# Optimization experiments

Hardware: AMD Instinct MI355X
Metric: run time of the kernel (lower is better)

The kernel has to match this reference:

```python
import jax, jax.numpy as jnp
import numpy as np

_SAMPLING_EPS = 1e-5
NEG_INF = jnp.float32(-jnp.inf)


def setup_inputs() -> dict:
    key = jax.random.key(0)
    k1, k2, k3, k4, k5 = jax.random.split(key, 5)
    B, V = 128, 128000
    logits = jax.random.normal(k1, (B, V), dtype=jnp.float32) * 4.0
    # every 8th row is greedy (temperature 0), rest random in [0.1, 1.5)
    rand_t = 0.1 + 1.4 * jax.random.uniform(k2, (B,), dtype=jnp.float32)
    temperatures = jnp.where(jnp.arange(B) % 8 == 0, 0.0, rand_t)
    top_k = jax.random.randint(k3, (B,), 1, 1001, dtype=jnp.int64)
    top_p = 0.1 + 0.9 * jax.random.uniform(k4, (B,), dtype=jnp.float32)
    # q ~ Exponential(1), replaces torch's generator-based q.exponential_()
    exp_noise = jax.random.exponential(k5, (B, V), dtype=jnp.float32)
    return {"logits": logits, "temperatures": temperatures, "top_k": top_k,
            "top_p": top_p, "exp_noise": exp_noise}


def _masked_logits(logits, temperatures, top_k, top_p):
    B, V = logits.shape
    # apply_temperature: greedy rows (temp < eps) divide by 1.0
    temp = jnp.where(temperatures < _SAMPLING_EPS, 1.0, temperatures)
    x = logits / temp[:, None]                       # [B, V]
    # ascending sort (as in torch code)
    sort_idx = jnp.argsort(x, axis=-1)               # [B, V]
    x_sort = jnp.take_along_axis(x, sort_idx, axis=-1)
    # top-k: keep the k largest (last k of ascending sort)
    k = jnp.clip(top_k, None, V).astype(jnp.int32)
    thr_idx = (V - k)[:, None]                       # [B, 1]
    thr = jnp.take_along_axis(x_sort, thr_idx, axis=-1)
    x_sort = jnp.where(x_sort < thr, NEG_INF, x_sort)
    # top-p on the sorted (ascending) logits
    probs_sort = jax.nn.softmax(x_sort, axis=-1)
    probs_sum = jnp.cumsum(probs_sort, axis=-1)
    p_mask = probs_sum <= (1.0 - top_p)[:, None]
    p_mask = p_mask.at[:, -1].set(False)             # always keep the max
    x_sort = jnp.where(p_mask, NEG_INF, x_sort)
    # scatter back to original positions: out[b, sort_idx[b, j]] = x_sort[b, j]
    rows = jnp.arange(B)[:, None]
    return x.at[rows, sort_idx].set(x_sort)


def reference(logits, temperatures, top_k, top_p, exp_noise):
    logits = logits.astype(jnp.float32)
    greedy = jnp.argmax(logits, axis=-1)             # [B]
    masked = _masked_logits(logits, temperatures, top_k, top_p)
    probs = jax.nn.softmax(masked, axis=-1)
    # Gumbel-max / exponential-race sampling: argmax(probs / q)
    random_sampled = jnp.argmax(probs / exp_noise, axis=-1)
    sampled = jnp.where(temperatures < _SAMPLING_EPS, greedy, random_sampled)
    return sampled[:, None].astype(jnp.int32)        # SamplerOutput.sampled_token_ids
```

## Files before the change

kernel.cpp:

```cpp
#include <hip/hip_runtime.h>
#include <stdint.h>

#define HB 4096
#define CAP 4096
#define SL1 5
#define SL3 20
#define THR1 256
#define THR4 1024
#define SEPS 1e-5f
#define ZMAX 8
#define LBUF 2048

typedef unsigned long long ull;

__device__ __forceinline__ uint32_t f2key(float x) {
  uint32_t u = __float_as_uint(x);
  return u ^ ((u & 0x80000000u) ? 0xFFFFFFFFu : 0x80000000u);
}
__device__ __forceinline__ float key2f(uint32_t k) {
  uint32_t u = (k & 0x80000000u) ? (k ^ 0x80000000u) : ~k;
  return __uint_as_float(u);
}

__global__ void k1_hist(const float* __restrict__ logits, const float* __restrict__ noise,
                        const float* __restrict__ temps,
                        unsigned int* __restrict__ hist, ull* __restrict__ rowmax,
                        unsigned int* __restrict__ zcnt, int* __restrict__ zlist,
                        int V, int slice_len) {
  __shared__ unsigned int h[HB];
  __shared__ ull s_w64[THR1 / 64];
  int tid = threadIdx.x;
  int row = blockIdx.x / SL1;
  int slice = blockIdx.x % SL1;
  for (int b = tid; b < HB; b += THR1) h[b] = 0;
  __syncthreads();
  float tr = temps[row];
  float te = (tr < SEPS) ? 1.0f : tr;
  int col_base = slice * slice_len;
  const float4* p4 = reinterpret_cast<const float4*>(logits + (size_t)row * V + col_base);
  const float4* q4 = reinterpret_cast<const float4*>(noise + (size_t)row * V + col_base);
  int n4 = slice_len >> 2;
  ull best = 0ULL;
  for (int v = tid; v < n4; v += THR1) {
    float4 f = p4[v];
    float4 q = q4[v];
    int c0 = col_base + 4 * v;
    float xs[4] = {f.x, f.y, f.z, f.w};
    float qs[4] = {q.x, q.y, q.z, q.w};
#pragma unroll
    for (int m = 0; m < 4; ++m) {
      float x = xs[m] / te;
      uint32_t key = f2key(x);
      if (key >= 0x80000000u)
        atomicAdd(&h[(key & 0x7FFFFFFFu) >> 19], 1u);
      ull pk = ((ull)key << 32) | (ull)(uint32_t)(V - 1 - (c0 + m));
      if (pk > best) best = pk;
      if (qs[m] == 0.0f) {
        unsigned int p = atomicAdd(&zcnt[row], 1u);
        if (p < ZMAX) zlist[row * ZMAX + p] = c0 + m;
      }
    }
  }
  for (int off = 32; off > 0; off >>= 1) {
    ull o = __shfl_down(best, off);
    if (o > best) best = o;
  }
  int lane = tid & 63, wid = tid >> 6;
  if (lane == 0) s_w64[wid] = best;
  __syncthreads();
  if (tid == 0) {
    ull b2 = s_w64[0];
    for (int w = 1; w < THR1 / 64; ++w) if (s_w64[w] > b2) b2 = s_w64[w];
    atomicMax(&rowmax[row], b2);
  }
  for (int b = tid; b < HB; b += THR1) {
    unsigned int c = h[b];
    if (c) atomicAdd(&hist[(size_t)row * HB + b], c);
  }
}

__global__ void k2_select(const unsigned int* __restrict__ hist, const int* __restrict__ topk32,
                          unsigned int* __restrict__ tcap, int* __restrict__ kks, int B, int V) {
  __shared__ int s_flag;
  __shared__ unsigned int s_scan[256];
  int tid = threadIdx.x, row = blockIdx.x;
  if (tid == 0) { s_flag = 0; tcap[row] = 0x80000000u; }
  __syncthreads();
  if (tid < B && topk32[tid] == 0) s_flag = 1;
  __syncthreads();
  int kraw = s_flag ? topk32[2 * row] : topk32[row];
  int kk = kraw < 1 ? 1 : (kraw > V ? V : kraw);
  if (tid == 0) kks[row] = kk;
  unsigned int h[16];
  unsigned int csum = 0;
  const unsigned int* hr = hist + (size_t)row * HB;
#pragma unroll
  for (int c = 0; c < 16; ++c) { h[c] = hr[tid * 16 + c]; csum += h[c]; }
  s_scan[tid] = csum;
  __syncthreads();
  for (int off = 1; off < 256; off <<= 1) {
    unsigned int v = s_scan[tid];
    unsigned int u = (tid + off < 256) ? s_scan[tid + off] : 0u;
    __syncthreads();
    s_scan[tid] = v + u;
    __syncthreads();
  }
  unsigned int run = (tid < 255) ? s_scan[tid + 1] : 0u;
  for (int c = 15; c >= 0; --c) {
    unsigned int prev = run;
    run += h[c];
    if (run >= (unsigned int)kk && prev < (unsigned int)kk)
      tcap[row] = 0x80000000u | ((unsigned int)(tid * 16 + c) << 19);
  }
}

__global__ void k3_capture(const float* __restrict__ logits, const float* __restrict__ temps,
                           const unsigned int* __restrict__ tcap,
                           ull* __restrict__ cand, unsigned int* __restrict__ cnt,
                           int V, int slice_len) {
  __shared__ ull s_buf[LBUF];
  __shared__ unsigned int s_n, s_base;
  int tid = threadIdx.x;
  int row = blockIdx.x / SL3;
  int slice = blockIdx.x % SL3;
  if (tid == 0) s_n = 0;
  __syncthreads();
  float tr = temps[row];
  float te = (tr < SEPS) ? 1.0f : tr;
  unsigned int tk = tcap[row];
  int col_base = slice * slice_len;
  const float4* p4 = reinterpret_cast<const float4*>(logits + (size_t)row * V + col_base);
  int n4 = slice_len >> 2;
  for (int v = tid; v < n4; v += THR1) {
    float4 f = p4[v];
    int c0 = col_base + 4 * v;
    float xs[4] = {f.x, f.y, f.z, f.w};
#pragma unroll
    for (int m = 0; m < 4; ++m) {
      uint32_t key = f2key(xs[m] / te);
      if (key >= tk) {
        ull pk = ((ull)key << 32) | (ull)(uint32_t)(c0 + m);
        unsigned int pos = atomicAdd(&s_n, 1u);
        if (pos < LBUF) s_buf[pos] = pk;
        else {
          unsigned int g = atomicAdd(&cnt[row], 1u);
          if (g < CAP) cand[(size_t)row * CAP + g] = pk;
        }
      }
    }
  }
  __syncthreads();
  unsigned int m = (s_n < LBUF) ? s_n : LBUF;
  if (tid == 0) s_base = atomicAdd(&cnt[row], m);
  __syncthreads();
  unsigned int base = s_base;
  for (unsigned int i = tid; i < m; i += THR1) {
    unsigned int g = base + i;
    if (g < CAP) cand[(size_t)row * CAP + g] = s_buf[i];
  }
}

__global__ __launch_bounds__(THR4) void k4_final(
    const ull* __restrict__ cand, const unsigned int* __restrict__ cnt,
    const int* __restrict__ kks, const float* __restrict__ temps,
    const float* __restrict__ topp, const float* __restrict__ noise,
    const ull* __restrict__ rowmax, const unsigned int* __restrict__ zcnt,
    const int* __restrict__ zlist, int* __restrict__ out, int V) {
  __shared__ ull s_cand[CAP];
  __shared__ float s_e[CAP];
  __shared__ unsigned char s_kept[CAP];
  __shared__ float s_w[16];
  __shared__ ull s_w64[16];
  __shared__ int s_nan, s_pz;
  int tid = threadIdx.x, row = blockIdx.x;
  int lane = tid & 63, wid = tid >> 6;
  if (tid == 0) s_nan = 0x7FFFFFFF;
  unsigned int cv = cnt[row];
  int n = (cv < (unsigned int)CAP) ? (int)cv : CAP;
  if (n < 1) n = 1;
  int N = 64;
  while (N < n) N <<= 1;
  for (int i = tid; i < N; i += THR4)
    s_cand[i] = (i < n) ? cand[(size_t)row * CAP + i] : 0ULL;
  __syncthreads();
  for (int k = 2; k <= 64; k <<= 1) {
    for (int j = k >> 1; j > 0; j >>= 1) {
      for (int i = tid; i < N; i += THR4) {
        int l = i ^ j;
        if (l > i) {
          ull a = s_cand[i], b = s_cand[l];
          bool up = ((i & k) == 0);
          if (up ? (a < b) : (a > b)) { s_cand[i] = b; s_cand[l] = a; }
        }
      }
      __builtin_amdgcn_wave_barrier();
    }
  }
  __syncthreads();
  for (int k = 128; k <= N; k <<= 1) {
    for (int j = k >> 1; j >= 64; j >>= 1) {
      for (int i = tid; i < N; i += THR4) {
        int l = i ^ j;
        if (l > i) {
          ull a = s_cand[i], b = s_cand[l];
          bool up = ((i & k) == 0);
          if (up ? (a < b) : (a > b)) { s_cand[i] = b; s_cand[l] = a; }
        }
      }
      __syncthreads();
    }
    for (int j = 32; j > 0; j >>= 1) {
      for (int i = tid; i < N; i += THR4) {
        int l = i ^ j;
        if (l > i) {
          ull a = s_cand[i], b = s_cand[l];
          bool up = ((i & k) == 0);
          if (up ? (a < b) : (a > b)) { s_cand[i] = b; s_cand[l] = a; }
        }
      }
      __builtin_amdgcn_wave_barrier();
    }
    __syncthreads();
  }
  int kk = kks[row];
  if (kk > n) kk = n;
  uint32_t thrkey = (uint32_t)(s_cand[kk - 1] >> 32);
  float xmax = key2f((uint32_t)(s_cand[0] >> 32));
  int C = N / THR4;
  if (C < 1) C = 1;
  int i0 = tid * C;
  float csum = 0.f;
  for (int c = 0; c < C; ++c) {
    int i = i0 + c;
    if (i < N) {
      uint32_t key = (uint32_t)(s_cand[i] >> 32);
      float e = 0.f;
      if (i < n && key >= thrkey) e = expf(key2f(key) - xmax);
      s_e[i] = e;
      csum += e;
    }
  }
  {
    float v = csum;
    for (int off = 32; off > 0; off >>= 1) v += __shfl_xor(v, off);
    if (lane == 0) s_w[wid] = v;
  }
  __syncthreads();
  float Z1 = 0.f;
  for (int w = 0; w < 16; ++w) Z1 += s_w[w];
  float pcsum = 0.f;
  for (int c = 0; c < C; ++c) {
    int i = i0 + c;
    if (i < N) pcsum += s_e[i] / Z1;
  }
  float sfx = pcsum;
  for (int off = 1; off < 64; off <<= 1) {
    float o = __shfl_down(sfx, off);
    if (lane + off < 64) sfx += o;
  }
  __syncthreads();
  if (lane == 0) s_w[wid] = sfx;
  __syncthreads();
  float above = sfx - pcsum;
  for (int w = wid + 1; w < 16; ++w) above += s_w[w];
  float thresh = 1.0f - topp[row];
  float run = above, z2 = 0.f;
  for (int c = C - 1; c >= 0; --c) {
    int i = i0 + c;
    if (i < N) {
      run += s_e[i] / Z1;
      uint32_t key = (uint32_t)(s_cand[i] >> 32);
      bool kept = (i < n) && (key >= thrkey) && (run > thresh || i == 0);
      s_kept[i] = kept ? 1 : 0;
      if (kept) z2 += s_e[i];
    }
  }
  {
    float v = z2;
    for (int off = 32; off > 0; off >>= 1) v += __shfl_xor(v, off);
    __syncthreads();
    if (lane == 0) s_w[wid] = v;
  }
  __syncthreads();
  float Z2 = 0.f;
  for (int w = 0; w < 16; ++w) Z2 += s_w[w];
  unsigned int nzc = zcnt[row];
  int nz = (nzc < (unsigned int)ZMAX) ? (int)nzc : ZMAX;
  for (int zi = 0; zi < nz; ++zi) {
    int z = zlist[row * ZMAX + zi];
    if (tid == 0) s_pz = 0;
    __syncthreads();
    for (int c = 0; c < C; ++c) {
      int i = i0 + c;
      if (i < n && (int)(uint32_t)(s_cand[i] & 0xFFFFFFFFu) == z && s_kept[i] && s_e[i] > 0.f)
        s_pz = 1;
    }
    __syncthreads();
    if (tid == 0 && s_pz == 0 && z < s_nan) s_nan = z;
    __syncthreads();
  }
  const float* qrow = noise + (size_t)row * V;
  ull pk = 0ULL;
  for (int c = 0; c < C; ++c) {
    int i = i0 + c;
    if (i < N && s_kept[i]) {
      int idx = (int)(uint32_t)(s_cand[i] & 0xFFFFFFFFu);
      float r = (s_e[i] / Z2) / qrow[idx];
      ull p = ((ull)__float_as_uint(r) << 32) |
              (ull)(0xFFFFFFFFu - (uint32_t)idx);
      if (p > pk) pk = p;
    }
  }
  for (int off = 32; off > 0; off >>= 1) {
    ull o = __shfl_xor(pk, off);
    if (o > pk) pk = o;
  }
  if (lane == 0) s_w64[wid] = pk;
  __syncthreads();
  if (tid == 0) {
    ull best = s_w64[0];
    for (int w = 1; w < 16; ++w) if (s_w64[w] > best) best = s_w64[w];
    int winner = (int)(0xFFFFFFFFu - (uint32_t)(best & 0xFFFFFFFFu));
    if (s_nan != 0x7FFFFFFF) winner = s_nan;
    ull rm = rowmax[row];
    int greedy = V - 1 - (int)(uint32_t)(rm & 0xFFFFFFFFu);
    out[row] = (temps[row] < SEPS) ? greedy : winner;
  }
}

extern "C" void kernel_launch(void* const* d_in, const int* in_sizes, int n_in,
                              void* d_out, int out_size, void* d_ws, size_t ws_size,
                              hipStream_t stream) {
  const float* logits = (const float*)d_in[0];
  const float* temps  = (const float*)d_in[1];
  const int*   topk   = (const int*)d_in[2];
  const float* topp   = (const float*)d_in[3];
  const float* noise  = (const float*)d_in[4];
  int B = in_sizes[1];
  int V = in_sizes[0] / B;
  int slice1 = V / SL1;
  int slice3 = V / SL3;

  char* ws = (char*)d_ws;
  size_t off = 0;
  ull* cand = (ull*)(ws + off); off += (size_t)B * CAP * 8;
  size_t zstart = off;
  ull* rowmax = (ull*)(ws + off); off += (size_t)B * 8;
  unsigned int* hist = (unsigned int*)(ws + off); off += (size_t)B * HB * 4;
  unsigned int* tcap = (unsigned int*)(ws + off); off += (size_t)B * 4;
  int* kks = (int*)(ws + off); off += (size_t)B * 4;
  unsigned int* cnt = (unsigned int*)(ws + off); off += (size_t)B * 4;
  unsigned int* zcnt = (unsigned int*)(ws + off); off += (size_t)B * 4;
  size_t zend = off;
  int* zlist = (int*)(ws + off); off += (size_t)B * ZMAX * 4;

  hipMemsetAsync(ws + zstart, 0, zend - zstart, stream);
  k1_hist<<<dim3(B * SL1), dim3(THR1), 0, stream>>>(logits, noise, temps, hist, rowmax,
                                                    zcnt, zlist, V, slice1);
  k2_select<<<dim3(B), dim3(256), 0, stream>>>(hist, topk, tcap, kks, B, V);
  k3_capture<<<dim3(B * SL3), dim3(THR1), 0, stream>>>(logits, temps, tcap, cand, cnt, V, slice3);
  k4_final<<<dim3(B), dim3(THR4), 0, stream>>>(cand, cnt, kks, temps, topp, noise, rowmax,
                                               zcnt, zlist, (int*)d_out, V);
}
```

Measured before the change: 209.5 us.

## Split greedy and sampled rows, histogram raw logits, move noise scan to capture

Greedy rows now only compute the argmax in the histogram kernel and exit early in the capture and final kernels. Sampled rows skip the argmax and build the histogram on raw logits, since dividing by a positive temperature preserves order. The temperature division is applied only to the captured candidates in the final kernel. The zero-noise scan moves from the histogram pass to the capture pass, so the first pass reads half as much data, and the first pass is split into four times as many blocks. The trade-off is that the capture pass now streams the noise array as well.

```diff
diff --git a/kernel.cpp b/kernel.cpp
--- a/kernel.cpp
+++ b/kernel.cpp
@@ -3,7 +3,7 @@
 
 #define HB 4096
 #define CAP 4096
-#define SL1 5
+#define SL1 20
 #define SL3 20
 #define THR1 256
 #define THR4 1024
@@ -22,57 +22,59 @@
   return __uint_as_float(u);
 }
 
-__global__ void k1_hist(const float* __restrict__ logits, const float* __restrict__ noise,
-                        const float* __restrict__ temps,
+__global__ void k1_hist(const float* __restrict__ logits, const float* __restrict__ temps,
                         unsigned int* __restrict__ hist, ull* __restrict__ rowmax,
-                        unsigned int* __restrict__ zcnt, int* __restrict__ zlist,
                         int V, int slice_len) {
   __shared__ unsigned int h[HB];
   __shared__ ull s_w64[THR1 / 64];
   int tid = threadIdx.x;
   int row = blockIdx.x / SL1;
   int slice = blockIdx.x % SL1;
-  for (int b = tid; b < HB; b += THR1) h[b] = 0;
-  __syncthreads();
   float tr = temps[row];
-  float te = (tr < SEPS) ? 1.0f : tr;
   int col_base = slice * slice_len;
   const float4* p4 = reinterpret_cast<const float4*>(logits + (size_t)row * V + col_base);
-  const float4* q4 = reinterpret_cast<const float4*>(noise + (size_t)row * V + col_base);
   int n4 = slice_len >> 2;
-  ull best = 0ULL;
+
+  if (tr < SEPS) {
+    ull best = 0ULL;
+    for (int v = tid; v < n4; v += THR1) {
+      float4 f = p4[v];
+      int c0 = col_base + 4 * v;
+      float xs[4] = {f.x, f.y, f.z, f.w};
+#pragma unroll
+      for (int m = 0; m < 4; ++m) {
+        ull pk = ((ull)f2key(xs[m]) << 32) | (ull)(uint32_t)(V - 1 - (c0 + m));
+        if (pk > best) best = pk;
+      }
+    }
+    for (int off = 32; off > 0; off >>= 1) {
+      ull o = __shfl_down(best, off);
+      if (o > best) best = o;
+    }
+    int lane = tid & 63, wid = tid >> 6;
+    if (lane == 0) s_w64[wid] = best;
+    __syncthreads();
+    if (tid == 0) {
+      ull b2 = s_w64[0];
+      for (int w = 1; w < THR1 / 64; ++w) if (s_w64[w] > b2) b2 = s_w64[w];
+      atomicMax(&rowmax[row], b2);
+    }
+    return;
+  }
+
+  for (int b = tid; b < HB; b += THR1) h[b] = 0;
+  __syncthreads();
   for (int v = tid; v < n4; v += THR1) {
     float4 f = p4[v];
-    float4 q = q4[v];
-    int c0 = col_base + 4 * v;
     float xs[4] = {f.x, f.y, f.z, f.w};
-    float qs[4] = {q.x, q.y, q.z, q.w};
 #pragma unroll
     for (int m = 0; m < 4; ++m) {
-      float x = xs[m] / te;
-      uint32_t key = f2key(x);
+      uint32_t key = f2key(xs[m]);
       if (key >= 0x80000000u)
         atomicAdd(&h[(key & 0x7FFFFFFFu) >> 19], 1u);
-      ull pk = ((ull)key << 32) | (ull)(uint32_t)(V - 1 - (c0 + m));
-      if (pk > best) best = pk;
-      if (qs[m] == 0.0f) {
-        unsigned int p = atomicAdd(&zcnt[row], 1u);
-        if (p < ZMAX) zlist[row * ZMAX + p] = c0 + m;
-      }
-    }
-  }
-  for (int off = 32; off > 0; off >>= 1) {
-    ull o = __shfl_down(best, off);
-    if (o > best) best = o;
-  }
-  int lane = tid & 63, wid = tid >> 6;
-  if (lane == 0) s_w64[wid] = best;
-  __syncthreads();
-  if (tid == 0) {
-    ull b2 = s_w64[0];
-    for (int w = 1; w < THR1 / 64; ++w) if (s_w64[w] > b2) b2 = s_w64[w];
-    atomicMax(&rowmax[row], b2);
-  }
+    }
+  }
+  __syncthreads();
   for (int b = tid; b < HB; b += THR1) {
     unsigned int c = h[b];
     if (c) atomicAdd(&hist[(size_t)row * HB + b], c);
@@ -114,30 +116,33 @@
   }
 }
 
-__global__ void k3_capture(const float* __restrict__ logits, const float* __restrict__ temps,
-                           const unsigned int* __restrict__ tcap,
+__global__ void k3_capture(const float* __restrict__ logits, const float* __restrict__ noise,
+                           const float* __restrict__ temps, const unsigned int* __restrict__ tcap,
                            ull* __restrict__ cand, unsigned int* __restrict__ cnt,
+                           unsigned int* __restrict__ zcnt, int* __restrict__ zlist,
                            int V, int slice_len) {
   __shared__ ull s_buf[LBUF];
   __shared__ unsigned int s_n, s_base;
   int tid = threadIdx.x;
   int row = blockIdx.x / SL3;
   int slice = blockIdx.x % SL3;
+  if (temps[row] < SEPS) return;
   if (tid == 0) s_n = 0;
   __syncthreads();
-  float tr = temps[row];
-  float te = (tr < SEPS) ? 1.0f : tr;
   unsigned int tk = tcap[row];
   int col_base = slice * slice_len;
   const float4* p4 = reinterpret_cast<const float4*>(logits + (size_t)row * V + col_base);
+  const float4* q4 = reinterpret_cast<const float4*>(noise + (size_t)row * V + col_base);
   int n4 = slice_len >> 2;
   for (int v = tid; v < n4; v += THR1) {
     float4 f = p4[v];
+    float4 q = q4[v];
     int c0 = col_base + 4 * v;
     float xs[4] = {f.x, f.y, f.z, f.w};
+    float qs[4] = {q.x, q.y, q.z, q.w};
 #pragma unroll
     for (int m = 0; m < 4; ++m) {
-      uint32_t key = f2key(xs[m] / te);
+      uint32_t key = f2key(xs[m]);
       if (key >= tk) {
         ull pk = ((ull)key << 32) | (ull)(uint32_t)(c0 + m);
         unsigned int pos = atomicAdd(&s_n, 1u);
@@ -146,6 +151,10 @@
           unsigned int g = atomicAdd(&cnt[row], 1u);
           if (g < CAP) cand[(size_t)row * CAP + g] = pk;
         }
+      }
+      if (qs[m] == 0.0f) {
+        unsigned int p = atomicAdd(&zcnt[row], 1u);
+        if (p < ZMAX) zlist[row * ZMAX + p] = c0 + m;
       }
     }
   }
@@ -174,14 +183,29 @@
   __shared__ int s_nan, s_pz;
   int tid = threadIdx.x, row = blockIdx.x;
   int lane = tid & 63, wid = tid >> 6;
+  float tr = temps[row];
+  if (tr < SEPS) {
+    if (tid == 0) {
+      ull rm = rowmax[row];
+      out[row] = V - 1 - (int)(uint32_t)(rm & 0xFFFFFFFFu);
+    }
+    return;
+  }
   if (tid == 0) s_nan = 0x7FFFFFFF;
   unsigned int cv = cnt[row];
   int n = (cv < (unsigned int)CAP) ? (int)cv : CAP;
   if (n < 1) n = 1;
   int N = 64;
   while (N < n) N <<= 1;
-  for (int i = tid; i < N; i += THR4)
-    s_cand[i] = (i < n) ? cand[(size_t)row * CAP + i] : 0ULL;
+  for (int i = tid; i < N; i += THR4) {
+    ull pk = 0ULL;
+    if (i < n) {
+      ull c = cand[(size_t)row * CAP + i];
+      float x = key2f((uint32_t)(c >> 32)) / tr;
+      pk = ((ull)f2key(x) << 32) | (c & 0xFFFFFFFFu);
+    }
+    s_cand[i] = pk;
+  }
   __syncthreads();
   for (int k = 2; k <= 64; k <<= 1) {
     for (int j = k >> 1; j > 0; j >>= 1) {
@@ -322,9 +346,7 @@
     for (int w = 1; w < 16; ++w) if (s_w64[w] > best) best = s_w64[w];
     int winner = (int)(0xFFFFFFFFu - (uint32_t)(best & 0xFFFFFFFFu));
     if (s_nan != 0x7FFFFFFF) winner = s_nan;
-    ull rm = rowmax[row];
-    int greedy = V - 1 - (int)(uint32_t)(rm & 0xFFFFFFFFu);
-    out[row] = (temps[row] < SEPS) ? greedy : winner;
+    out[row] = winner;
   }
 }
 
@@ -355,10 +377,10 @@
   int* zlist = (int*)(ws + off); off += (size_t)B * ZMAX * 4;
 
   hipMemsetAsync(ws + zstart, 0, zend - zstart, stream);
-  k1_hist<<<dim3(B * SL1), dim3(THR1), 0, stream>>>(logits, noise, temps, hist, rowmax,
-                                                    zcnt, zlist, V, slice1);
+  k1_hist<<<dim3(B * SL1), dim3(THR1), 0, stream>>>(logits, temps, hist, rowmax, V, slice1);
   k2_select<<<dim3(B), dim3(256), 0, stream>>>(hist, topk, tcap, kks, B, V);
-  k3_capture<<<dim3(B * SL3), dim3(THR1), 0, stream>>>(logits, temps, tcap, cand, cnt, V, slice3);
+  k3_capture<<<dim3(B * SL3), dim3(THR1), 0, stream>>>(logits, noise, temps, tcap, cand, cnt,
+                                                       zcnt, zlist, V, slice3);
   k4_final<<<dim3(B), dim3(THR4), 0, stream>>>(cand, cnt, kks, temps, topp, noise, rowmax,
                                                zcnt, zlist, (int*)d_out, V);
 }
```

Measured after the change: 200.8 us. -4.2%, faster.
